# Performance work log

Hardware: AMD Instinct MI355X
Metric: run time of the kernel (lower is better)

Reference implementation:

```python
import jax, jax.numpy as jnp
import numpy as np

BLOCK_SIZE = 32
EPS = 1e-6


def setup_inputs() -> dict:
    key = jax.random.key(0)
    k1, k2, k3, k4, k5 = jax.random.split(key, 5)
    B, H, L, D = 2, 16, 4096, 128
    return {
        "query_states": jax.random.normal(k1, (B, H, L, D), dtype=jnp.float32),
        "key_states": jax.random.normal(k2, (B, H, L, D), dtype=jnp.float32),
        "value_states": jax.random.normal(k3, (B, H, L, D), dtype=jnp.float32),
        # learned params; init near torch defaults (ones/zeros) with small noise
        "phi_scale": 1.0 + 0.1 * jax.random.normal(k4, (H, 1, D), dtype=jnp.float32),
        "phi_bias": 0.1 * jax.random.normal(k5, (H, 1, D), dtype=jnp.float32),
    }


def _forward(query_states, key_states, value_states, phi_scale, phi_bias):
    B, H, L, D = query_states.shape
    bs = BLOCK_SIZE
    N = L // bs  # L chosen divisible by block_size (no padding path)

    def feature_map(x):  # x: (B,H,N,bs,D)
        # phi_scale (H,1,D) -> (H,1,1,D) broadcasts over (B,H,N,bs,D)
        y = jax.nn.elu(x * phi_scale[:, None] + phi_bias[:, None]) + 1.0
        return jnp.clip(y, 0.0, 10.0)

    q = query_states.reshape(B, H, N, bs, D)
    k = key_states.reshape(B, H, N, bs, D)
    v = value_states.reshape(B, H, N, bs, D)

    phi_q = feature_map(q)
    phi_k = feature_map(k)

    # move block axis to front for scan: (N,B,H,bs,D)
    pq = jnp.moveaxis(phi_q, 2, 0)
    pk = jnp.moveaxis(phi_k, 2, 0)
    vb = jnp.moveaxis(v, 2, 0)

    S0 = jnp.zeros((B, H, D, D), dtype=jnp.float32)
    Z0 = jnp.zeros((B, H, D), dtype=jnp.float32)

    def step(carry, inp):
        S, Z = carry
        pq_n, pk_n, v_n = inp  # each (B,H,bs,D)
        # block-causal, bidirectional within block: update state BEFORE output
        S = S + jnp.einsum('bhkd,bhke->bhde', pk_n, v_n)
        Z = Z + pk_n.sum(axis=-2)
        num = jnp.einsum('bhqd,bhde->bhqe', pq_n, S)
        den = jnp.maximum(jnp.einsum('bhqd,bhd->bhq', pq_n, Z), EPS)
        return (S, Z), num / den[..., None]

    _, out_blocks = jax.lax.scan(step, (S0, Z0), (pq, pk, vb))  # (N,B,H,bs,D)
    out = jnp.moveaxis(out_blocks, 0, 2).reshape(B, H, L, D)
    return out


def reference(query_states, key_states, value_states, phi_scale, phi_bias):
    return _forward(query_states, key_states, value_states, phi_scale, phi_bias)
```

## Files before the change

kernel.cpp:

```cpp
#include <hip/hip_runtime.h>
#include <stdint.h>

#define BH 32
#define LSEQ 4096
#define DDIM 128
#define BS 32
#define NBLK 128
#define CHUNKS 16
#define BLK_PER_CHUNK 8
#define STATE_SZ (DDIM*DDIM + DDIM)

typedef __attribute__((ext_vector_type(8))) short bf16x8;
typedef __attribute__((ext_vector_type(4))) float f32x4;

__device__ inline uint16_t f2bf(float f) {
    uint32_t x = __builtin_bit_cast(uint32_t, f);
    x += 0x7fffu + ((x >> 16) & 1u);
    return (uint16_t)(x >> 16);
}
__device__ inline float bflo(uint32_t w){ return __builtin_bit_cast(float, w << 16); }
__device__ inline float bfhi(uint32_t w){ return __builtin_bit_cast(float, w & 0xffff0000u); }

__device__ inline float phi_f(float x, float s, float b) {
    float y = fmaf(x, s, b);
    float pos = fminf(y + 1.0f, 10.0f);
    float neg = __expf(y);
    return (y > 0.0f) ? pos : neg;
}

__device__ inline void bar_lgkm() {
    asm volatile("s_waitcnt lgkmcnt(0)\n\ts_barrier" ::: "memory");
}

#define SMEM_BYTES 57984

template<bool PHASE2>
__global__ __launch_bounds__(512, 4) void la_phase(
    const float* __restrict__ Q, const float* __restrict__ K,
    const float* __restrict__ V, const float* __restrict__ scale,
    const float* __restrict__ bias, float* __restrict__ states,
    float* __restrict__ out)
{
    extern __shared__ char smem[];
    uint16_t* pkT    = (uint16_t*)smem;
    uint16_t* pq_bf  = (uint16_t*)smem;
    uint16_t* vT     = (uint16_t*)(smem + 10240);
    uint16_t* S_bfT  = (uint16_t*)(smem + 20480);
    float* Zl        = (float*)(smem + 55296);
    float* Zpart     = Zl + 128;
    float* inv_den   = Zpart + 4*128;

    const int tid  = threadIdx.x;
    const int bid  = blockIdx.x;
    const int bh   = bid >> 4;
    const int ch   = bid & 15;
    const int lane = tid & 63;
    const int wv   = tid >> 6;
    const int i15  = lane & 15;
    const int q4   = lane >> 4;

    const size_t base = (size_t)bh * LSEQ * DDIM;
    const int h = bh & 15;

    const int kd = tid & 127;
    const int rg = tid >> 7;
    const int sr = tid >> 4;
    const int sc = (tid & 15) * 8;

    const float sk = scale[h*DDIM + kd];
    const float bk = bias [h*DDIM + kd];
    float sreg[8], breg[8];
    if (PHASE2) {
        #pragma unroll
        for (int j = 0; j < 8; ++j) {
            sreg[j] = scale[h*DDIM + sc + j];
            breg[j] = bias [h*DDIM + sc + j];
        }
    }

    f32x4 accS[8];
    float* stbase = states + (size_t)(bh*CHUNKS + ch) * STATE_SZ;

    if (PHASE2) {
        #pragma unroll
        for (int mt = 0; mt < 8; ++mt) {
            #pragma unroll
            for (int r = 0; r < 4; ++r) {
                int d = 16*mt + 4*q4 + r;
                accS[mt][r] = stbase[d*DDIM + 16*wv + i15];
            }
        }
        if (tid < 128) Zl[tid] = stbase[DDIM*DDIM + tid];
    } else {
        #pragma unroll
        for (int mt = 0; mt < 8; ++mt) accS[mt] = (f32x4){0.f,0.f,0.f,0.f};
        if (tid < 128) Zl[tid] = 0.f;
    }
    __syncthreads();

    float kreg[8], vreg[8], qreg[8];
    {
        const size_t coff = base + (size_t)((ch*BLK_PER_CHUNK)*BS + 8*rg)*DDIM + kd;
        #pragma unroll
        for (int j = 0; j < 8; ++j) {
            kreg[j] = K[coff + (size_t)j*DDIM];
            vreg[j] = V[coff + (size_t)j*DDIM];
        }
        if (PHASE2) {
            const size_t qoff = base + (size_t)((ch*BLK_PER_CHUNK)*BS + sr)*DDIM + sc;
            const float4 a0 = *(const float4*)(Q + qoff);
            const float4 a1 = *(const float4*)(Q + qoff + 4);
            qreg[0]=a0.x; qreg[1]=a0.y; qreg[2]=a0.z; qreg[3]=a0.w;
            qreg[4]=a1.x; qreg[5]=a1.y; qreg[6]=a1.z; qreg[7]=a1.w;
        }
    }

    for (int s = 0; s < BLK_PER_CHUNK; ++s) {
        const int blk = ch * BLK_PER_CHUNK + s;

        {
            uint32_t pk[4], pv[4];
            float zp = 0.f;
            #pragma unroll
            for (int j = 0; j < 4; ++j) {
                uint32_t lo = f2bf(phi_f(kreg[2*j],   sk, bk));
                uint32_t hi = f2bf(phi_f(kreg[2*j+1], sk, bk));
                pk[j] = lo | (hi << 16);
                zp += bflo(lo) + bflo(hi);
                uint32_t vlo = f2bf(vreg[2*j]);
                uint32_t vhi = f2bf(vreg[2*j+1]);
                pv[j] = vlo | (vhi << 16);
            }
            *(uint4*)&pkT[kd*40 + 8*rg] = *(uint4*)pk;
            *(uint4*)&vT [kd*40 + 8*rg] = *(uint4*)pv;
            Zpart[rg*128 + kd] = zp;
        }
        if (s + 1 < BLK_PER_CHUNK) {
            const size_t coff = base + (size_t)((blk+1)*BS + 8*rg)*DDIM + kd;
            #pragma unroll
            for (int j = 0; j < 8; ++j) {
                kreg[j] = K[coff + (size_t)j*DDIM];
                vreg[j] = V[coff + (size_t)j*DDIM];
            }
        }
        bar_lgkm();

        if (tid < 128) {
            float z = Zl[tid];
            #pragma unroll
            for (int g = 0; g < 4; ++g) z += Zpart[g*128 + tid];
            Zl[tid] = z;
        }
        {
            bf16x8 bv = *(const bf16x8*)&vT[(16*wv + i15)*40 + 8*q4];
            __builtin_amdgcn_s_setprio(1);
            #pragma unroll
            for (int mt = 0; mt < 8; ++mt) {
                bf16x8 av = *(const bf16x8*)&pkT[(16*mt + i15)*40 + 8*q4];
                accS[mt] = __builtin_amdgcn_mfma_f32_16x16x32_bf16(av, bv, accS[mt], 0, 0, 0);
            }
            __builtin_amdgcn_s_setprio(0);
        }

        if (PHASE2) {
            bar_lgkm();

            {
                uint32_t pq[4];
                #pragma unroll
                for (int j = 0; j < 4; ++j) {
                    uint32_t lo = f2bf(phi_f(qreg[2*j],   sreg[2*j],   breg[2*j]));
                    uint32_t hi = f2bf(phi_f(qreg[2*j+1], sreg[2*j+1], breg[2*j+1]));
                    pq[j] = lo | (hi << 16);
                }
                *(uint4*)&pq_bf[sr*136 + sc] = *(uint4*)pq;
                float sden = 0.f;
                #pragma unroll
                for (int j = 0; j < 4; ++j)
                    sden += bflo(pq[j]) * Zl[sc + 2*j] + bfhi(pq[j]) * Zl[sc + 2*j + 1];
                #pragma unroll
                for (int off = 1; off < 16; off <<= 1)
                    sden += __shfl_xor(sden, off, 64);
                if ((tid & 15) == 0) inv_den[sr] = 1.0f / fmaxf(sden, 1e-6f);
            }
            #pragma unroll
            for (int mt = 0; mt < 8; ++mt) {
                uint2 o;
                o.x = (uint32_t)f2bf(accS[mt][0]) | ((uint32_t)f2bf(accS[mt][1]) << 16);
                o.y = (uint32_t)f2bf(accS[mt][2]) | ((uint32_t)f2bf(accS[mt][3]) << 16);
                *(uint2*)&S_bfT[(16*wv + i15)*136 + 16*mt + 4*q4] = o;
            }
            if (s + 1 < BLK_PER_CHUNK) {
                const size_t qoff = base + (size_t)((blk+1)*BS + sr)*DDIM + sc;
                const float4 a0 = *(const float4*)(Q + qoff);
                const float4 a1 = *(const float4*)(Q + qoff + 4);
                qreg[0]=a0.x; qreg[1]=a0.y; qreg[2]=a0.z; qreg[3]=a0.w;
                qreg[4]=a1.x; qreg[5]=a1.y; qreg[6]=a1.z; qreg[7]=a1.w;
            }
            bar_lgkm();

            f32x4 acc2[2];
            acc2[0] = (f32x4){0.f,0.f,0.f,0.f};
            acc2[1] = (f32x4){0.f,0.f,0.f,0.f};
            __builtin_amdgcn_s_setprio(1);
            #pragma unroll
            for (int ks = 0; ks < 4; ++ks) {
                bf16x8 sb = *(const bf16x8*)&S_bfT[(16*wv + i15)*136 + 32*ks + 8*q4];
                #pragma unroll
                for (int qt = 0; qt < 2; ++qt) {
                    bf16x8 qa = *(const bf16x8*)&pq_bf[(16*qt + i15)*136 + 32*ks + 8*q4];
                    acc2[qt] = __builtin_amdgcn_mfma_f32_16x16x32_bf16(qa, sb, acc2[qt], 0, 0, 0);
                }
            }
            __builtin_amdgcn_s_setprio(0);
            bar_lgkm();

            #pragma unroll
            for (int qt = 0; qt < 2; ++qt) {
                #pragma unroll
                for (int r = 0; r < 4; ++r) {
                    int qrow = 16*qt + 4*q4 + r;
                    float o = acc2[qt][r] * inv_den[qrow];
                    out[base + (size_t)(blk*BS + qrow)*DDIM + 16*wv + i15] = o;
                }
            }
        } else {
            bar_lgkm();
        }
    }

    if (!PHASE2) {
        #pragma unroll
        for (int mt = 0; mt < 8; ++mt) {
            #pragma unroll
            for (int r = 0; r < 4; ++r) {
                int d = 16*mt + 4*q4 + r;
                stbase[d*DDIM + 16*wv + i15] = accS[mt][r];
            }
        }
        if (tid < 128) stbase[DDIM*DDIM + tid] = Zl[tid];
    }
}

__global__ void la_prefix(float* __restrict__ states) {
    const int bh = blockIdx.x >> 4;
    const int sl = blockIdx.x & 15;
    const int slice = STATE_SZ / 16;
    float* p0 = states + (size_t)bh * CHUNKS * STATE_SZ + sl * slice;
    for (int i = threadIdx.x; i < slice; i += 256) {
        float run = 0.f;
        float* p = p0 + i;
        #pragma unroll
        for (int c = 0; c < CHUNKS; ++c) {
            float v = p[(size_t)c * STATE_SZ];
            p[(size_t)c * STATE_SZ] = run;
            run += v;
        }
    }
}

extern "C" void kernel_launch(void* const* d_in, const int* in_sizes, int n_in,
                              void* d_out, int out_size, void* d_ws, size_t ws_size,
                              hipStream_t stream) {
    const float* Q     = (const float*)d_in[0];
    const float* K     = (const float*)d_in[1];
    const float* V     = (const float*)d_in[2];
    const float* scale = (const float*)d_in[3];
    const float* bias  = (const float*)d_in[4];
    float* out    = (float*)d_out;
    float* states = (float*)d_ws;

    hipLaunchKernelGGL((la_phase<false>), dim3(BH*CHUNKS), dim3(512), SMEM_BYTES, stream,
                       Q, K, V, scale, bias, states, out);
    hipLaunchKernelGGL(la_prefix, dim3(BH*16), dim3(256), 0, stream, states);
    hipLaunchKernelGGL((la_phase<true>), dim3(BH*CHUNKS), dim3(512), SMEM_BYTES, stream,
                       Q, K, V, scale, bias, states, out);
}
```

Baseline: 275.3 us.

## Rewrite chunked linear attention with intra-chunk masked QK^T and swizzled LDS

Replaces the per-32-row sequential state update in the output phase with a chunk-level formulation. Each chunk computes phi(Q)·S_prefix once, then adds block-causal intra-chunk attention via phi(Q)phi(K)^T tiles, masked per block, times V. The state pass now processes 64-row groups with double-buffered, XOR-swizzled LDS, and the prefix kernel is re-gridded. This removes the repeated state bf16 re-materialisation and the many barriers per 32-row block, at the cost of more LDS and lower occupancy in the forward kernel.

After: 306.5 us. +11.4%, slower.

```diff
diff --git a/kernel.cpp b/kernel.cpp
--- a/kernel.cpp
+++ b/kernel.cpp
@@ -4,10 +4,8 @@
 #define BH 32
 #define LSEQ 4096
 #define DDIM 128
-#define BS 32
-#define NBLK 128
 #define CHUNKS 16
-#define BLK_PER_CHUNK 8
+#define CHUNK_ROWS 256
 #define STATE_SZ (DDIM*DDIM + DDIM)
 
 typedef __attribute__((ext_vector_type(8))) short bf16x8;
@@ -18,244 +16,333 @@
     x += 0x7fffu + ((x >> 16) & 1u);
     return (uint16_t)(x >> 16);
 }
-__device__ inline float bflo(uint32_t w){ return __builtin_bit_cast(float, w << 16); }
-__device__ inline float bfhi(uint32_t w){ return __builtin_bit_cast(float, w & 0xffff0000u); }
-
+__device__ inline uint32_t pack2(float a, float b) {
+    return (uint32_t)f2bf(a) | ((uint32_t)f2bf(b) << 16);
+}
 __device__ inline float phi_f(float x, float s, float b) {
     float y = fmaf(x, s, b);
     float pos = fminf(y + 1.0f, 10.0f);
     float neg = __expf(y);
     return (y > 0.0f) ? pos : neg;
 }
-
 __device__ inline void bar_lgkm() {
     asm volatile("s_waitcnt lgkmcnt(0)\n\ts_barrier" ::: "memory");
 }
 
-#define SMEM_BYTES 57984
-
-template<bool PHASE2>
-__global__ __launch_bounds__(512, 4) void la_phase(
+#define SMEM1 67584
+__global__ __launch_bounds__(512, 4) void la_state(
+    const float* __restrict__ K, const float* __restrict__ V,
+    const float* __restrict__ scale, const float* __restrict__ bias,
+    float* __restrict__ states)
+{
+    extern __shared__ char smem[];
+    const int tid  = threadIdx.x;
+    const int bh   = blockIdx.x >> 4;
+    const int ch   = blockIdx.x & 15;
+    const int h    = bh & 15;
+    const int lane = tid & 63;
+    const int wid  = tid >> 6;
+    const int i15  = lane & 15;
+    const int q4   = lane >> 4;
+    const size_t base = (size_t)bh * LSEQ * DDIM;
+    const int row0 = ch * CHUNK_ROWS;
+
+    const int d  = tid & 127;
+    const int rg = tid >> 7;
+    const float sk = scale[h*DDIM + d];
+    const float bk = bias [h*DDIM + d];
+
+    f32x4 accS[8];
+    #pragma unroll
+    for (int mt = 0; mt < 8; ++mt) accS[mt] = (f32x4){0.f,0.f,0.f,0.f};
+    float zacc = 0.f;
+
+    float kreg[16], vreg[16];
+    auto load_kv = [&](int g) {
+        const float* Kc = K + base + (size_t)(row0 + 64*g + 16*rg)*DDIM + d;
+        const float* Vc = V + base + (size_t)(row0 + 64*g + 16*rg)*DDIM + d;
+        #pragma unroll
+        for (int j = 0; j < 16; ++j) {
+            kreg[j] = Kc[(size_t)j*DDIM];
+            vreg[j] = Vc[(size_t)j*DDIM];
+        }
+    };
+    auto stage = [&](int b) {
+        uint32_t wk[8], wv8[8];
+        #pragma unroll
+        for (int j = 0; j < 8; ++j) {
+            float p0 = phi_f(kreg[2*j],   sk, bk);
+            float p1 = phi_f(kreg[2*j+1], sk, bk);
+            zacc += p0 + p1;
+            wk[j]  = pack2(p0, p1);
+            wv8[j] = pack2(vreg[2*j], vreg[2*j+1]);
+        }
+        char* pkb = smem + b*16384;
+        char* vtb = smem + 32768 + b*16384;
+        const uint32_t lin = (uint32_t)(d*128 + 32*rg);
+        const uint32_t swz = (uint32_t)((d & 7) << 4);
+        *(uint4*)(pkb + ((lin     ) ^ swz)) = ((const uint4*)wk)[0];
+        *(uint4*)(pkb + ((lin + 16) ^ swz)) = ((const uint4*)wk)[1];
+        *(uint4*)(vtb + ((lin     ) ^ swz)) = ((const uint4*)wv8)[0];
+        *(uint4*)(vtb + ((lin + 16) ^ swz)) = ((const uint4*)wv8)[1];
+    };
+
+    load_kv(0);
+    stage(0);
+    load_kv(1);
+    bar_lgkm();
+
+    #pragma unroll
+    for (int g = 0; g < 4; ++g) {
+        if (g < 3) stage((g+1)&1);
+        if (g < 2) load_kv(g+2);
+        const char* pkb = smem + (g&1)*16384;
+        const char* vtb = smem + 32768 + (g&1)*16384;
+        const uint32_t swz = (uint32_t)((i15 & 7) << 4);
+        #pragma unroll
+        for (int ksl = 0; ksl < 2; ++ksl) {
+            bf16x8 bv = *(const bf16x8*)(vtb + (((uint32_t)((16*wid+i15)*128 + 64*ksl + 16*q4)) ^ swz));
+            #pragma unroll
+            for (int mt = 0; mt < 8; ++mt) {
+                bf16x8 av = *(const bf16x8*)(pkb + (((uint32_t)((16*mt+i15)*128 + 64*ksl + 16*q4)) ^ swz));
+                accS[mt] = __builtin_amdgcn_mfma_f32_16x16x32_bf16(av, bv, accS[mt], 0, 0, 0);
+            }
+        }
+        bar_lgkm();
+    }
+
+    float* Zpart = (float*)(smem + 65536);
+    Zpart[rg*128 + d] = zacc;
+    float* stb = states + (size_t)(bh*CHUNKS + ch)*STATE_SZ;
+    #pragma unroll
+    for (int mt = 0; mt < 8; ++mt)
+        #pragma unroll
+        for (int r = 0; r < 4; ++r)
+            stb[(size_t)(16*mt + 4*q4 + r)*DDIM + 16*wid + i15] = accS[mt][r];
+    bar_lgkm();
+    if (tid < 128)
+        stb[DDIM*DDIM + tid] = Zpart[tid] + Zpart[128+tid] + Zpart[256+tid] + Zpart[384+tid];
+}
+
+__global__ void la_prefix(float* __restrict__ states) {
+    const int bh  = blockIdx.y;
+    const int idx = blockIdx.x * 128 + threadIdx.x;
+    float* p = states + (size_t)bh * CHUNKS * STATE_SZ + idx;
+    float run = 0.f;
+    #pragma unroll
+    for (int c = 0; c < CHUNKS; ++c) {
+        float v = p[(size_t)c * STATE_SZ];
+        p[(size_t)c * STATE_SZ] = run;
+        run += v;
+    }
+}
+
+#define SMEM2 119808
+__global__ __launch_bounds__(512, 2) void la_fwd(
     const float* __restrict__ Q, const float* __restrict__ K,
     const float* __restrict__ V, const float* __restrict__ scale,
-    const float* __restrict__ bias, float* __restrict__ states,
+    const float* __restrict__ bias, const float* __restrict__ states,
     float* __restrict__ out)
 {
     extern __shared__ char smem[];
-    uint16_t* pkT    = (uint16_t*)smem;
-    uint16_t* pq_bf  = (uint16_t*)smem;
-    uint16_t* vT     = (uint16_t*)(smem + 10240);
-    uint16_t* S_bfT  = (uint16_t*)(smem + 20480);
-    float* Zl        = (float*)(smem + 55296);
-    float* Zpart     = Zl + 128;
-    float* inv_den   = Zpart + 4*128;
-
     const int tid  = threadIdx.x;
-    const int bid  = blockIdx.x;
-    const int bh   = bid >> 4;
-    const int ch   = bid & 15;
+    const int bh   = blockIdx.x >> 4;
+    const int ch   = blockIdx.x & 15;
+    const int h    = bh & 15;
     const int lane = tid & 63;
-    const int wv   = tid >> 6;
+    const int wid  = tid >> 6;
     const int i15  = lane & 15;
     const int q4   = lane >> 4;
-
     const size_t base = (size_t)bh * LSEQ * DDIM;
-    const int h = bh & 15;
-
-    const int kd = tid & 127;
-    const int rg = tid >> 7;
-    const int sr = tid >> 4;
-    const int sc = (tid & 15) * 8;
-
-    const float sk = scale[h*DDIM + kd];
-    const float bk = bias [h*DDIM + kd];
-    float sreg[8], breg[8];
-    if (PHASE2) {
-        #pragma unroll
-        for (int j = 0; j < 8; ++j) {
-            sreg[j] = scale[h*DDIM + sc + j];
-            breg[j] = bias [h*DDIM + sc + j];
-        }
-    }
-
-    f32x4 accS[8];
-    float* stbase = states + (size_t)(bh*CHUNKS + ch) * STATE_SZ;
-
-    if (PHASE2) {
-        #pragma unroll
-        for (int mt = 0; mt < 8; ++mt) {
+    const int row0 = ch * CHUNK_ROWS;
+    const float* stb = states + (size_t)(bh*CHUNKS + ch)*STATE_SZ;
+
+    const int krow = tid >> 3;
+    const int kd8  = (tid & 7) * 16;
+    const int ve   = tid & 127;
+    const int vrg  = tid >> 7;
+
+    float skr[16], bkr[16];
+    #pragma unroll
+    for (int u = 0; u < 4; ++u) {
+        *(float4*)&skr[4*u] = *(const float4*)(scale + h*DDIM + kd8 + 4*u);
+        *(float4*)&bkr[4*u] = *(const float4*)(bias  + h*DDIM + kd8 + 4*u);
+    }
+
+    float4 kq[4];
+    float  vr[16];
+    auto load_kv = [&](int g) {
+        const float* Kr = K + base + (size_t)(row0 + 64*g + krow)*DDIM + kd8;
+        #pragma unroll
+        for (int u = 0; u < 4; ++u) kq[u] = *(const float4*)(Kr + 4*u);
+        const float* Vc = V + base + (size_t)(row0 + 64*g + 16*vrg)*DDIM + ve;
+        #pragma unroll
+        for (int j = 0; j < 16; ++j) vr[j] = Vc[(size_t)j*DDIM];
+    };
+    auto stage_kv = [&](int b) {
+        char* pkb = smem + 32768 + b*32768;
+        char* vtb = pkb + 16384;
+        uint32_t wk[8];
+        #pragma unroll
+        for (int u = 0; u < 4; ++u) {
+            float x0 = phi_f(kq[u].x, skr[4*u+0], bkr[4*u+0]);
+            float x1 = phi_f(kq[u].y, skr[4*u+1], bkr[4*u+1]);
+            float x2 = phi_f(kq[u].z, skr[4*u+2], bkr[4*u+2]);
+            float x3 = phi_f(kq[u].w, skr[4*u+3], bkr[4*u+3]);
+            wk[2*u]   = pack2(x0, x1);
+            wk[2*u+1] = pack2(x2, x3);
+        }
+        uint32_t lin = (uint32_t)(krow*256 + kd8*2);
+        uint32_t swz = (uint32_t)((krow & 7) << 4);
+        *(uint4*)(pkb + ((lin     ) ^ swz)) = ((const uint4*)wk)[0];
+        *(uint4*)(pkb + ((lin + 16) ^ swz)) = ((const uint4*)wk)[1];
+        uint32_t wv8[8];
+        #pragma unroll
+        for (int j = 0; j < 8; ++j) wv8[j] = pack2(vr[2*j], vr[2*j+1]);
+        lin = (uint32_t)(ve*128 + 32*vrg);
+        swz = (uint32_t)((ve & 7) << 4);
+        *(uint4*)(vtb + ((lin     ) ^ swz)) = ((const uint4*)wv8)[0];
+        *(uint4*)(vtb + ((lin + 16) ^ swz)) = ((const uint4*)wv8)[1];
+    };
+
+    load_kv(0);
+
+    {
+        const int se  = tid & 127;
+        const int sdg = tid >> 7;
+        float sv[32];
+        const float* srcp = stb + (size_t)(32*sdg)*DDIM + se;
+        #pragma unroll
+        for (int k2 = 0; k2 < 32; ++k2) sv[k2] = srcp[(size_t)k2*DDIM];
+        uint32_t wbuf[16];
+        #pragma unroll
+        for (int k2 = 0; k2 < 16; ++k2) wbuf[k2] = pack2(sv[2*k2], sv[2*k2+1]);
+        const uint32_t linb = (uint32_t)(se*256 + 64*sdg);
+        const uint32_t swz  = (uint32_t)((se & 7) << 4);
+        #pragma unroll
+        for (int m = 0; m < 4; ++m)
+            *(uint4*)(smem + ((linb + 16*m) ^ swz)) = ((const uint4*)wbuf)[m];
+    }
+
+    stage_kv(0);
+    load_kv(1);
+
+    bf16x8 pq[2][4];
+    float dacc0 = 0.f, dacc1 = 0.f;
+    #pragma unroll
+    for (int ks = 0; ks < 4; ++ks) {
+        const float* sp = scale + h*DDIM + 32*ks + 8*q4;
+        const float* bp = bias  + h*DDIM + 32*ks + 8*q4;
+        const float* zp = stb + DDIM*DDIM + 32*ks + 8*q4;
+        float4 s0 = *(const float4*)sp, s1 = *(const float4*)(sp+4);
+        float4 b0 = *(const float4*)bp, b1 = *(const float4*)(bp+4);
+        float4 z0 = *(const float4*)zp, z1 = *(const float4*)(zp+4);
+        #pragma unroll
+        for (int qt = 0; qt < 2; ++qt) {
+            const float* qp = Q + base + (size_t)(row0 + 32*wid + 16*qt + i15)*DDIM + 32*ks + 8*q4;
+            float4 a0 = *(const float4*)qp, a1 = *(const float4*)(qp+4);
+            float f0 = phi_f(a0.x, s0.x, b0.x), f1 = phi_f(a0.y, s0.y, b0.y);
+            float f2 = phi_f(a0.z, s0.z, b0.z), f3 = phi_f(a0.w, s0.w, b0.w);
+            float f4 = phi_f(a1.x, s1.x, b1.x), f5 = phi_f(a1.y, s1.y, b1.y);
+            float f6 = phi_f(a1.z, s1.z, b1.z), f7 = phi_f(a1.w, s1.w, b1.w);
+            float ds = f0*z0.x + f1*z0.y + f2*z0.z + f3*z0.w
+                     + f4*z1.x + f5*z1.y + f6*z1.z + f7*z1.w;
+            if (qt == 0) dacc0 += ds; else dacc1 += ds;
+            uint4 uu = { pack2(f0,f1), pack2(f2,f3), pack2(f4,f5), pack2(f6,f7) };
+            pq[qt][ks] = __builtin_bit_cast(bf16x8, uu);
+        }
+    }
+
+    bar_lgkm();
+
+    f32x4 acc[2][8];
+    #pragma unroll
+    for (int qt = 0; qt < 2; ++qt)
+        #pragma unroll
+        for (int et = 0; et < 8; ++et) acc[qt][et] = (f32x4){0.f,0.f,0.f,0.f};
+    {
+        const uint32_t swz = (uint32_t)((i15 & 7) << 4);
+        #pragma unroll
+        for (int ks = 0; ks < 4; ++ks)
             #pragma unroll
-            for (int r = 0; r < 4; ++r) {
-                int d = 16*mt + 4*q4 + r;
-                accS[mt][r] = stbase[d*DDIM + 16*wv + i15];
+            for (int et = 0; et < 8; ++et) {
+                bf16x8 sb = *(const bf16x8*)(smem + (((uint32_t)((16*et+i15)*256 + 64*ks + 16*q4)) ^ swz));
+                acc[0][et] = __builtin_amdgcn_mfma_f32_16x16x32_bf16(pq[0][ks], sb, acc[0][et], 0, 0, 0);
+                acc[1][et] = __builtin_amdgcn_mfma_f32_16x16x32_bf16(pq[1][ks], sb, acc[1][et], 0, 0, 0);
             }
-        }
-        if (tid < 128) Zl[tid] = stbase[DDIM*DDIM + tid];
-    } else {
-        #pragma unroll
-        for (int mt = 0; mt < 8; ++mt) accS[mt] = (f32x4){0.f,0.f,0.f,0.f};
-        if (tid < 128) Zl[tid] = 0.f;
-    }
-    __syncthreads();
-
-    float kreg[8], vreg[8], qreg[8];
-    {
-        const size_t coff = base + (size_t)((ch*BLK_PER_CHUNK)*BS + 8*rg)*DDIM + kd;
-        #pragma unroll
-        for (int j = 0; j < 8; ++j) {
-            kreg[j] = K[coff + (size_t)j*DDIM];
-            vreg[j] = V[coff + (size_t)j*DDIM];
-        }
-        if (PHASE2) {
-            const size_t qoff = base + (size_t)((ch*BLK_PER_CHUNK)*BS + sr)*DDIM + sc;
-            const float4 a0 = *(const float4*)(Q + qoff);
-            const float4 a1 = *(const float4*)(Q + qoff + 4);
-            qreg[0]=a0.x; qreg[1]=a0.y; qreg[2]=a0.z; qreg[3]=a0.w;
-            qreg[4]=a1.x; qreg[5]=a1.y; qreg[6]=a1.z; qreg[7]=a1.w;
-        }
-    }
-
-    for (int s = 0; s < BLK_PER_CHUNK; ++s) {
-        const int blk = ch * BLK_PER_CHUNK + s;
-
-        {
-            uint32_t pk[4], pv[4];
-            float zp = 0.f;
-            #pragma unroll
-            for (int j = 0; j < 4; ++j) {
-                uint32_t lo = f2bf(phi_f(kreg[2*j],   sk, bk));
-                uint32_t hi = f2bf(phi_f(kreg[2*j+1], sk, bk));
-                pk[j] = lo | (hi << 16);
-                zp += bflo(lo) + bflo(hi);
-                uint32_t vlo = f2bf(vreg[2*j]);
-                uint32_t vhi = f2bf(vreg[2*j+1]);
-                pv[j] = vlo | (vhi << 16);
-            }
-            *(uint4*)&pkT[kd*40 + 8*rg] = *(uint4*)pk;
-            *(uint4*)&vT [kd*40 + 8*rg] = *(uint4*)pv;
-            Zpart[rg*128 + kd] = zp;
-        }
-        if (s + 1 < BLK_PER_CHUNK) {
-            const size_t coff = base + (size_t)((blk+1)*BS + 8*rg)*DDIM + kd;
-            #pragma unroll
-            for (int j = 0; j < 8; ++j) {
-                kreg[j] = K[coff + (size_t)j*DDIM];
-                vreg[j] = V[coff + (size_t)j*DDIM];
-            }
-        }
-        bar_lgkm();
-
-        if (tid < 128) {
-            float z = Zl[tid];
-            #pragma unroll
-            for (int g = 0; g < 4; ++g) z += Zpart[g*128 + tid];
-            Zl[tid] = z;
-        }
-        {
-            bf16x8 bv = *(const bf16x8*)&vT[(16*wv + i15)*40 + 8*q4];
-            __builtin_amdgcn_s_setprio(1);
-            #pragma unroll
-            for (int mt = 0; mt < 8; ++mt) {
-                bf16x8 av = *(const bf16x8*)&pkT[(16*mt + i15)*40 + 8*q4];
-                accS[mt] = __builtin_amdgcn_mfma_f32_16x16x32_bf16(av, bv, accS[mt], 0, 0, 0);
-            }
-            __builtin_amdgcn_s_setprio(0);
-        }
-
-        if (PHASE2) {
-            bar_lgkm();
-
-            {
-                uint32_t pq[4];
+    }
+
+    #pragma unroll
+    for (int it = 0; it < 4; ++it) {
+        if (it < 3) stage_kv((it+1)&1);
+        if (it < 2) load_kv(it+2);
+        const char* pkb = smem + 32768 + (it&1)*32768;
+        const char* vtb = pkb + 16384;
+        const uint32_t swz = (uint32_t)((i15 & 7) << 4);
+        #pragma unroll
+        for (int tl = 0; tl < 2; ++tl) {
+            const int t = 2*it + tl;
+            if (t <= wid) {
+                f32x4 Aacc[2][2];
                 #pragma unroll
-                for (int j = 0; j < 4; ++j) {
-                    uint32_t lo = f2bf(phi_f(qreg[2*j],   sreg[2*j],   breg[2*j]));
-                    uint32_t hi = f2bf(phi_f(qreg[2*j+1], sreg[2*j+1], breg[2*j+1]));
-                    pq[j] = lo | (hi << 16);
+                for (int rt = 0; rt < 2; ++rt)
+                    #pragma unroll
+                    for (int qt = 0; qt < 2; ++qt) Aacc[rt][qt] = (f32x4){0.f,0.f,0.f,0.f};
+                #pragma unroll
+                for (int ks = 0; ks < 4; ++ks) {
+                    bf16x8 ak0 = *(const bf16x8*)(pkb + (((uint32_t)((32*tl      + i15)*256 + 64*ks + 16*q4)) ^ swz));
+                    bf16x8 ak1 = *(const bf16x8*)(pkb + (((uint32_t)((32*tl + 16 + i15)*256 + 64*ks + 16*q4)) ^ swz));
+                    Aacc[0][0] = __builtin_amdgcn_mfma_f32_16x16x32_bf16(ak0, pq[0][ks], Aacc[0][0], 0, 0, 0);
+                    Aacc[0][1] = __builtin_amdgcn_mfma_f32_16x16x32_bf16(ak0, pq[1][ks], Aacc[0][1], 0, 0, 0);
+                    Aacc[1][0] = __builtin_amdgcn_mfma_f32_16x16x32_bf16(ak1, pq[0][ks], Aacc[1][0], 0, 0, 0);
+                    Aacc[1][1] = __builtin_amdgcn_mfma_f32_16x16x32_bf16(ak1, pq[1][ks], Aacc[1][1], 0, 0, 0);
                 }
-                *(uint4*)&pq_bf[sr*136 + sc] = *(uint4*)pq;
-                float sden = 0.f;
+                dacc0 += Aacc[0][0][0]+Aacc[0][0][1]+Aacc[0][0][2]+Aacc[0][0][3]
+                       + Aacc[1][0][0]+Aacc[1][0][1]+Aacc[1][0][2]+Aacc[1][0][3];
+                dacc1 += Aacc[0][1][0]+Aacc[0][1][1]+Aacc[0][1][2]+Aacc[0][1][3]
+                       + Aacc[1][1][0]+Aacc[1][1][1]+Aacc[1][1][2]+Aacc[1][1][3];
+                char* al = smem + 98304 + wid*2560;
                 #pragma unroll
-                for (int j = 0; j < 4; ++j)
-                    sden += bflo(pq[j]) * Zl[sc + 2*j] + bfhi(pq[j]) * Zl[sc + 2*j + 1];
+                for (int rt = 0; rt < 2; ++rt)
+                    #pragma unroll
+                    for (int qt = 0; qt < 2; ++qt) {
+                        uint2 o;
+                        o.x = pack2(Aacc[rt][qt][0], Aacc[rt][qt][1]);
+                        o.y = pack2(Aacc[rt][qt][2], Aacc[rt][qt][3]);
+                        *(uint2*)(al + (uint32_t)(((16*qt + i15)*40 + 16*rt + 4*q4)*2)) = o;
+                    }
+                bf16x8 aq0 = *(const bf16x8*)(al + (uint32_t)((      i15*40 + 8*q4)*2));
+                bf16x8 aq1 = *(const bf16x8*)(al + (uint32_t)(((16 + i15)*40 + 8*q4)*2));
                 #pragma unroll
-                for (int off = 1; off < 16; off <<= 1)
-                    sden += __shfl_xor(sden, off, 64);
-                if ((tid & 15) == 0) inv_den[sr] = 1.0f / fmaxf(sden, 1e-6f);
-            }
-            #pragma unroll
-            for (int mt = 0; mt < 8; ++mt) {
-                uint2 o;
-                o.x = (uint32_t)f2bf(accS[mt][0]) | ((uint32_t)f2bf(accS[mt][1]) << 16);
-                o.y = (uint32_t)f2bf(accS[mt][2]) | ((uint32_t)f2bf(accS[mt][3]) << 16);
-                *(uint2*)&S_bfT[(16*wv + i15)*136 + 16*mt + 4*q4] = o;
-            }
-            if (s + 1 < BLK_PER_CHUNK) {
-                const size_t qoff = base + (size_t)((blk+1)*BS + sr)*DDIM + sc;
-                const float4 a0 = *(const float4*)(Q + qoff);
-                const float4 a1 = *(const float4*)(Q + qoff + 4);
-                qreg[0]=a0.x; qreg[1]=a0.y; qreg[2]=a0.z; qreg[3]=a0.w;
-                qreg[4]=a1.x; qreg[5]=a1.y; qreg[6]=a1.z; qreg[7]=a1.w;
-            }
-            bar_lgkm();
-
-            f32x4 acc2[2];
-            acc2[0] = (f32x4){0.f,0.f,0.f,0.f};
-            acc2[1] = (f32x4){0.f,0.f,0.f,0.f};
-            __builtin_amdgcn_s_setprio(1);
-            #pragma unroll
-            for (int ks = 0; ks < 4; ++ks) {
-                bf16x8 sb = *(const bf16x8*)&S_bfT[(16*wv + i15)*136 + 32*ks + 8*q4];
-                #pragma unroll
-                for (int qt = 0; qt < 2; ++qt) {
-                    bf16x8 qa = *(const bf16x8*)&pq_bf[(16*qt + i15)*136 + 32*ks + 8*q4];
-                    acc2[qt] = __builtin_amdgcn_mfma_f32_16x16x32_bf16(qa, sb, acc2[qt], 0, 0, 0);
+                for (int et = 0; et < 8; ++et) {
+                    bf16x8 bvv = *(const bf16x8*)(vtb + (((uint32_t)((16*et+i15)*128 + 64*tl + 16*q4)) ^ swz));
+                    acc[0][et] = __builtin_amdgcn_mfma_f32_16x16x32_bf16(aq0, bvv, acc[0][et], 0, 0, 0);
+                    acc[1][et] = __builtin_amdgcn_mfma_f32_16x16x32_bf16(aq1, bvv, acc[1][et], 0, 0, 0);
                 }
             }
-            __builtin_amdgcn_s_setprio(0);
-            bar_lgkm();
-
+        }
+        bar_lgkm();
+    }
+
+    dacc0 += __shfl_xor(dacc0, 16, 64); dacc0 += __shfl_xor(dacc0, 32, 64);
+    dacc1 += __shfl_xor(dacc1, 16, 64); dacc1 += __shfl_xor(dacc1, 32, 64);
+    float* denl = (float*)(smem + 118784);
+    if (q4 == 0) {
+        denl[wid*32 + i15]      = dacc0;
+        denl[wid*32 + 16 + i15] = dacc1;
+    }
+    #pragma unroll
+    for (int qt = 0; qt < 2; ++qt) {
+        float inv[4];
+        #pragma unroll
+        for (int r = 0; r < 4; ++r)
+            inv[r] = 1.0f / fmaxf(denl[wid*32 + 16*qt + 4*q4 + r], 1e-6f);
+        #pragma unroll
+        for (int et = 0; et < 8; ++et)
             #pragma unroll
-            for (int qt = 0; qt < 2; ++qt) {
-                #pragma unroll
-                for (int r = 0; r < 4; ++r) {
-                    int qrow = 16*qt + 4*q4 + r;
-                    float o = acc2[qt][r] * inv_den[qrow];
-                    out[base + (size_t)(blk*BS + qrow)*DDIM + 16*wv + i15] = o;
-                }
-            }
-        } else {
-            bar_lgkm();
-        }
-    }
-
-    if (!PHASE2) {
-        #pragma unroll
-        for (int mt = 0; mt < 8; ++mt) {
-            #pragma unroll
-            for (int r = 0; r < 4; ++r) {
-                int d = 16*mt + 4*q4 + r;
-                stbase[d*DDIM + 16*wv + i15] = accS[mt][r];
-            }
-        }
-        if (tid < 128) stbase[DDIM*DDIM + tid] = Zl[tid];
-    }
-}
-
-__global__ void la_prefix(float* __restrict__ states) {
-    const int bh = blockIdx.x >> 4;
-    const int sl = blockIdx.x & 15;
-    const int slice = STATE_SZ / 16;
-    float* p0 = states + (size_t)bh * CHUNKS * STATE_SZ + sl * slice;
-    for (int i = threadIdx.x; i < slice; i += 256) {
-        float run = 0.f;
-        float* p = p0 + i;
-        #pragma unroll
-        for (int c = 0; c < CHUNKS; ++c) {
-            float v = p[(size_t)c * STATE_SZ];
-            p[(size_t)c * STATE_SZ] = run;
-            run += v;
-        }
+            for (int r = 0; r < 4; ++r)
+                out[base + (size_t)(row0 + 32*wid + 16*qt + 4*q4 + r)*DDIM + 16*et + i15] =
+                    acc[qt][et][r] * inv[r];
     }
 }
 
@@ -270,9 +357,18 @@
     float* out    = (float*)d_out;
     float* states = (float*)d_ws;
 
-    hipLaunchKernelGGL((la_phase<false>), dim3(BH*CHUNKS), dim3(512), SMEM_BYTES, stream,
+    static bool s_attr = false;
+    if (!s_attr) {
+        hipFuncSetAttribute(reinterpret_cast<const void*>(la_state),
+                            hipFuncAttributeMaxDynamicSharedMemorySize, SMEM1);
+        hipFuncSetAttribute(reinterpret_cast<const void*>(la_fwd),
+                            hipFuncAttributeMaxDynamicSharedMemorySize, SMEM2);
+        s_attr = true;
+    }
+
+    hipLaunchKernelGGL(la_state, dim3(BH*CHUNKS), dim3(512), SMEM1, stream,
+                       K, V, scale, bias, states);
+    hipLaunchKernelGGL(la_prefix, dim3(129, BH), dim3(128), 0, stream, states);
+    hipLaunchKernelGGL(la_fwd, dim3(BH*CHUNKS), dim3(512), SMEM2, stream,
                        Q, K, V, scale, bias, states, out);
-    hipLaunchKernelGGL(la_prefix, dim3(BH*16), dim3(256), 0, stream, states);
-    hipLaunchKernelGGL((la_phase<true>), dim3(BH*CHUNKS), dim3(512), SMEM_BYTES, stream,
-                       Q, K, V, scale, bias, states, out);
-}
+}
```
